# Optimization experiments

Measured on AMD Instinct MI355X. Metric: run time of the kernel, lower is better.

## Reference

```python
import jax, jax.numpy as jnp
import numpy as np

EPS = 1e-8
B, N, C, RBF = 2, 512, 32, 32  # batch, points (== neighbors), channels, rbf size
RI, RO, ORD = 3, 1, 3          # 2*rank_in+1, 2*rank_out+1, 2*order+1


def setup_inputs() -> dict:
    key = jax.random.key(0)
    k = jax.random.split(key, 5)
    tensor = jax.random.normal(k[0], (B, N, C, RI), dtype=jnp.float32)
    rbf = jax.random.uniform(k[1], (B, N, N, RBF), dtype=jnp.float32)
    rij = jax.random.normal(k[2], (B, N, N, 3), dtype=jnp.float32)
    # Radial MLP params: xavier-normal weights, zero biases (per Radial defaults)
    W1 = jax.random.normal(k[3], (C, RBF), dtype=jnp.float32) * float(np.sqrt(2.0 / (RBF + C)))
    W2 = jax.random.normal(k[4], (C, C), dtype=jnp.float32) * float(np.sqrt(2.0 / (C + C)))
    b1 = jnp.zeros((C,), jnp.float32)
    b2 = jnp.zeros((C,), jnp.float32)
    return dict(tensor=tensor, rbf=rbf, rij=rij, W1=W1, b1=b1, W2=W2, b2=b2)


def reference(tensor, rbf, rij, W1, b1, W2, b2):
    # Radial two-layer MLP applied per edge: [B,N,K,RBF] -> [B,N,K,C]
    hidden = jax.nn.relu(b1 + jnp.einsum('bnkl,ml->bnkm', rbf, W1))
    R = b2 + jnp.einsum('bnkl,ml->bnkm', hidden, W2)
    # Mask self/degenerate edges (order != 0): zero R where |rij| < EPS
    r2 = jnp.sum(rij * rij, axis=-1)                      # [B,N,K]
    R = jnp.where((jnp.sqrt(r2) < EPS)[..., None], jnp.zeros_like(R), R)
    # Spherical harmonic order 1: unit direction vectors (eps-stabilized norm)
    Y = rij / jnp.sqrt(jnp.maximum(r2, EPS))[..., None]   # [B,N,K,3]
    cg = jnp.eye(ORD, dtype=R.dtype).reshape(RO, ORD, RI)
    # Outer product radial x angular: [B,N,K,C,3]
    F_out = R[..., None] * Y[..., None, :]
    # Contract CG, filter, neighbor features; sums over neighbor axis c
    return jnp.einsum('ijk,abcdj,acdk->abdi', cg, F_out, tensor)  # [B,N,C,RO]
```

## Files before the change

### kernel.cpp

```cpp
#include <hip/hip_runtime.h>
#include <hip/hip_bf16.h>

using bf16x8 = __attribute__((ext_vector_type(8))) short;
using f32x4  = __attribute__((ext_vector_type(4))) float;
using f32x16 = __attribute__((ext_vector_type(16))) float;
using u32x4  = __attribute__((ext_vector_type(4))) unsigned;

constexpr int N_ = 512;

__device__ __forceinline__ unsigned pkbf(float lo, float hi) {
    unsigned a = (unsigned short)__builtin_bit_cast(short, __float2bfloat16(lo));
    unsigned b = (unsigned short)__builtin_bit_cast(short, __float2bfloat16(hi));
    return a | (b << 16);
}
__device__ __forceinline__ float bfhi2f(unsigned u) { return __builtin_bit_cast(float, u & 0xFFFF0000u); }
__device__ __forceinline__ float bflo2f(unsigned u) { return __builtin_bit_cast(float, u << 16); }
__device__ __forceinline__ void gl2lds16(const float* g, float* l) {
    __builtin_amdgcn_global_load_lds(
        (const __attribute__((address_space(1))) void*)g,
        (__attribute__((address_space(3))) void*)l, 16, 0, 0);
}

__global__ __launch_bounds__(256)
void pack_tensor(const float* __restrict__ tensor, unsigned* __restrict__ tw) {
    const int i = blockIdx.x * 256 + threadIdx.x;
    const float x = tensor[3 * i + 0];
    const float y = tensor[3 * i + 1];
    const float z = tensor[3 * i + 2];
    reinterpret_cast<uint2*>(tw)[i] = make_uint2(pkbf(x, y), pkbf(z, 0.f));
}

__global__ __launch_bounds__(256, 4)
void filter_D(const unsigned* __restrict__ tw,
              const float* __restrict__ rbf,
              const float* __restrict__ rij,
              const float* __restrict__ W1,
              const float* __restrict__ b1,
              const float* __restrict__ W2,
              const float* __restrict__ b2,
              float* __restrict__ out)
{
    const int bn   = blockIdx.x;
    const int b    = bn >> 9;
    const int tid  = threadIdx.x;
    const int lane = tid & 63;
    const int w    = tid >> 6;
    const int lam  = lane & 31;
    const int l5   = lane >> 5;

    __shared__ unsigned upk[N_][2];
    __shared__ float    red[4][32];

    const float* rij_bn = rij + (size_t)bn * (N_ * 3);
    const float* rbf_bn = rbf + (size_t)bn * (N_ * 32);
    const uint2* twb    = (const uint2*)tw + (size_t)b * (N_ * 32);

    #pragma unroll
    for (int t = 0; t < 2; ++t) {
        const int k = tid + t * 256;
        const float rx = rij_bn[3 * k + 0];
        const float ry = rij_bn[3 * k + 1];
        const float rz = rij_bn[3 * k + 2];
        const float r2 = rx * rx + ry * ry + rz * rz;
        const float inv = rsqrtf(fmaxf(r2, 1e-8f));
        const float sc = (r2 >= 1e-16f) ? inv : 0.f;
        upk[k][0] = pkbf(rx * sc, ry * sc);
        upk[k][1] = pkbf(rz * sc, 0.f);
    }

    bf16x8 W1b[2];
    {
        const float* p1 = W1 + lam * 32 + 8 * l5;
        const f32x4 a0 = ((const f32x4*)p1)[0], a1 = ((const f32x4*)p1)[1];
        const f32x4 a2 = ((const f32x4*)(p1 + 16))[0], a3 = ((const f32x4*)(p1 + 16))[1];
        #pragma unroll
        for (int e = 0; e < 4; ++e) {
            W1b[0][e]     = __builtin_bit_cast(short, __float2bfloat16(a0[e]));
            W1b[0][4 + e] = __builtin_bit_cast(short, __float2bfloat16(a1[e]));
            W1b[1][e]     = __builtin_bit_cast(short, __float2bfloat16(a2[e]));
            W1b[1][4 + e] = __builtin_bit_cast(short, __float2bfloat16(a3[e]));
        }
    }
    const float b1s = b1[lam];

    __syncthreads();

    f32x4 xa[2], xb[2], xc[2], xd[2];
    {
        const float* ap = rbf_bn + (size_t)(w * 128 + lam) * 32 + 8 * l5;
        xa[0] = ((const f32x4*)ap)[0];
        xb[0] = ((const f32x4*)ap)[1];
        xc[0] = ((const f32x4*)(ap + 16))[0];
        xd[0] = ((const f32x4*)(ap + 16))[1];
    }

    f32x16 G;
    #pragma unroll
    for (int i = 0; i < 16; ++i) G[i] = 0.f;
    float ssum = 0.f;

    #pragma unroll
    for (int j = 0; j < 4; ++j) {
        const int e0  = (w * 4 + j) * 32;
        const int cur = j & 1, nx = cur ^ 1;

        uint2 tv1[8], tv2[8];
        #pragma unroll
        for (int e = 0; e < 8; ++e) {
            const int k1 = e0 + 8 * l5 + e;
            tv1[e] = twb[k1 * 32 + lam];
            tv2[e] = twb[(k1 + 16) * 32 + lam];
        }

        bf16x8 X0, X1;
        #pragma unroll
        for (int e = 0; e < 4; ++e) {
            X0[e]     = __builtin_bit_cast(short, __float2bfloat16(xa[cur][e]));
            X0[4 + e] = __builtin_bit_cast(short, __float2bfloat16(xb[cur][e]));
            X1[e]     = __builtin_bit_cast(short, __float2bfloat16(xc[cur][e]));
            X1[4 + e] = __builtin_bit_cast(short, __float2bfloat16(xd[cur][e]));
        }
        if (j < 3) {
            const float* ap = rbf_bn + (size_t)(e0 + 32 + lam) * 32 + 8 * l5;
            xa[nx] = ((const f32x4*)ap)[0];
            xb[nx] = ((const f32x4*)ap)[1];
            xc[nx] = ((const f32x4*)(ap + 16))[0];
            xd[nx] = ((const f32x4*)(ap + 16))[1];
        }

        f32x16 h;
        #pragma unroll
        for (int i = 0; i < 16; ++i) h[i] = 0.f;
        h = __builtin_amdgcn_mfma_f32_32x32x16_bf16(X0, W1b[0], h, 0, 0, 0);
        h = __builtin_amdgcn_mfma_f32_32x32x16_bf16(X1, W1b[1], h, 0, 0, 0);

        unsigned P0, P1, P2, P3, P4, P5, P6, P7;
        {
            const float t0 = fmaxf(h[0] + b1s, 0.f),  t1v = fmaxf(h[1] + b1s, 0.f);
            const float t2v = fmaxf(h[2] + b1s, 0.f), t3 = fmaxf(h[3] + b1s, 0.f);
            const float t4 = fmaxf(h[4] + b1s, 0.f),  t5 = fmaxf(h[5] + b1s, 0.f);
            const float t6 = fmaxf(h[6] + b1s, 0.f),  t7 = fmaxf(h[7] + b1s, 0.f);
            const float t8 = fmaxf(h[8] + b1s, 0.f),  t9 = fmaxf(h[9] + b1s, 0.f);
            const float tA = fmaxf(h[10] + b1s, 0.f), tB = fmaxf(h[11] + b1s, 0.f);
            const float tC = fmaxf(h[12] + b1s, 0.f), tD = fmaxf(h[13] + b1s, 0.f);
            const float tE = fmaxf(h[14] + b1s, 0.f), tF = fmaxf(h[15] + b1s, 0.f);
            P0 = pkbf(t0, t1v); P1 = pkbf(t2v, t3);
            P2 = pkbf(t4, t5);  P3 = pkbf(t6, t7);
            P4 = pkbf(t8, t9);  P5 = pkbf(tA, tB);
            P6 = pkbf(tC, tD);  P7 = pkbf(tE, tF);
        }
        const unsigned Q0 = __shfl_xor(P0, 32, 64);
        const unsigned Q1 = __shfl_xor(P1, 32, 64);
        const unsigned Q2 = __shfl_xor(P2, 32, 64);
        const unsigned Q3 = __shfl_xor(P3, 32, 64);
        const unsigned Q4 = __shfl_xor(P4, 32, 64);
        const unsigned Q5 = __shfl_xor(P5, 32, 64);
        const unsigned Q6 = __shfl_xor(P6, 32, 64);
        const unsigned Q7 = __shfl_xor(P7, 32, 64);
        const bool lo = (l5 == 0);
        const u32x4 A1 = { lo ? P0 : Q2, lo ? P1 : Q3, lo ? Q0 : P2, lo ? Q1 : P3 };
        const u32x4 A2 = { lo ? P4 : Q6, lo ? P5 : Q7, lo ? Q4 : P6, lo ? Q5 : P7 };

        u32x4 B1d, B2d;
        float sp;
        #pragma unroll
        for (int e = 0; e < 8; ++e) {
            const int kl = 8 * l5 + e;
            const unsigned u0 = upk[e0 + kl][0], u1 = upk[e0 + kl][1];
            const float s = bflo2f(u0) * bflo2f(tv1[e].x) + bfhi2f(u0) * bfhi2f(tv1[e].x)
                          + bflo2f(u1) * bflo2f(tv1[e].y);
            ssum += s;
            if (e & 1) B1d[e >> 1] = pkbf(sp, s); else sp = s;
        }
        #pragma unroll
        for (int e = 0; e < 8; ++e) {
            const int kl = 16 + 8 * l5 + e;
            const unsigned u0 = upk[e0 + kl][0], u1 = upk[e0 + kl][1];
            const float s = bflo2f(u0) * bflo2f(tv2[e].x) + bfhi2f(u0) * bfhi2f(tv2[e].x)
                          + bflo2f(u1) * bflo2f(tv2[e].y);
            ssum += s;
            if (e & 1) B2d[e >> 1] = pkbf(sp, s); else sp = s;
        }

        G = __builtin_amdgcn_mfma_f32_32x32x16_bf16(
                __builtin_bit_cast(bf16x8, A1), __builtin_bit_cast(bf16x8, B1d), G, 0, 0, 0);
        G = __builtin_amdgcn_mfma_f32_32x32x16_bf16(
                __builtin_bit_cast(bf16x8, A2), __builtin_bit_cast(bf16x8, B2d), G, 0, 0, 0);
    }

    float p = 0.f;
    #pragma unroll
    for (int q = 0; q < 4; ++q) {
        const f32x4 wv = *(const f32x4*)(W2 + lam * 32 + 8 * q + 4 * l5);
        p += wv[0] * G[4 * q + 0] + wv[1] * G[4 * q + 1]
           + wv[2] * G[4 * q + 2] + wv[3] * G[4 * q + 3];
    }
    p    += __shfl_xor(p, 32, 64);
    ssum += __shfl_xor(ssum, 32, 64);
    const float o = p + b2[lam] * ssum;
    if (l5 == 0) red[w][lam] = o;
    __syncthreads();
    if (tid < 32)
        out[bn * 32 + tid] = red[0][tid] + red[1][tid] + red[2][tid] + red[3][tid];
}

__global__ __launch_bounds__(256, 4)
void filter_L(const float* __restrict__ tensor, const float* __restrict__ rbf,
              const float* __restrict__ rij, const float* __restrict__ W1,
              const float* __restrict__ b1, const float* __restrict__ W2,
              const float* __restrict__ b2, float* __restrict__ out)
{
    const int bn = blockIdx.x, b = bn >> 9, tid = threadIdx.x;
    const int lane = tid & 63, w = tid >> 6, lam = lane & 31, l5 = lane >> 5;
    __shared__ float Ts[4][3072];
    __shared__ unsigned upk[N_][2];
    __shared__ float red[4][32];
    const float* rij_bn = rij + (size_t)bn * (N_ * 3);
    const float* rbf_bn = rbf + (size_t)bn * (N_ * 32);
    const float* ten_b  = tensor + (size_t)b * (N_ * 32 * 3);
    #pragma unroll
    for (int t = 0; t < 2; ++t) {
        const int k = tid + t * 256;
        const float rx = rij_bn[3 * k], ry = rij_bn[3 * k + 1], rz = rij_bn[3 * k + 2];
        const float r2 = rx * rx + ry * ry + rz * rz;
        const float inv = rsqrtf(fmaxf(r2, 1e-8f));
        const float sc = (r2 >= 1e-16f) ? inv : 0.f;
        upk[k][0] = pkbf(rx * sc, ry * sc);
        upk[k][1] = pkbf(rz * sc, 0.f);
    }
    bf16x8 W1b[2];
    {
        const float* p1 = W1 + lam * 32 + 8 * l5;
        const f32x4 a0 = ((const f32x4*)p1)[0], a1 = ((const f32x4*)p1)[1];
        const f32x4 a2 = ((const f32x4*)(p1 + 16))[0], a3 = ((const f32x4*)(p1 + 16))[1];
        #pragma unroll
        for (int e = 0; e < 4; ++e) {
            W1b[0][e] = __builtin_bit_cast(short, __float2bfloat16(a0[e]));
            W1b[0][4 + e] = __builtin_bit_cast(short, __float2bfloat16(a1[e]));
            W1b[1][e] = __builtin_bit_cast(short, __float2bfloat16(a2[e]));
            W1b[1][4 + e] = __builtin_bit_cast(short, __float2bfloat16(a3[e]));
        }
    }
    const float b1s = b1[lam];
    __syncthreads();
    float* tsw = &Ts[w][0];
    f32x4 xa[2], xb[2], xc[2], xd[2];
    {
        const float* ap = rbf_bn + (size_t)(w * 128 + lam) * 32 + 8 * l5;
        xa[0] = ((const f32x4*)ap)[0]; xb[0] = ((const f32x4*)ap)[1];
        xc[0] = ((const f32x4*)(ap + 16))[0]; xd[0] = ((const f32x4*)(ap + 16))[1];
    }
    {
        const float* gsrc = ten_b + (size_t)(w * 128) * 96;
        #pragma unroll
        for (int it = 0; it < 12; ++it) gl2lds16(gsrc + it * 256 + lane * 4, tsw + it * 256);
    }
    f32x16 G;
    #pragma unroll
    for (int i = 0; i < 16; ++i) G[i] = 0.f;
    float ssum = 0.f;
    #pragma unroll
    for (int j = 0; j < 4; ++j) {
        const int e0 = (w * 4 + j) * 32, cur = j & 1, nx = cur ^ 1;
        bf16x8 X0, X1;
        #pragma unroll
        for (int e = 0; e < 4; ++e) {
            X0[e] = __builtin_bit_cast(short, __float2bfloat16(xa[cur][e]));
            X0[4 + e] = __builtin_bit_cast(short, __float2bfloat16(xb[cur][e]));
            X1[e] = __builtin_bit_cast(short, __float2bfloat16(xc[cur][e]));
            X1[4 + e] = __builtin_bit_cast(short, __float2bfloat16(xd[cur][e]));
        }
        if (j < 3) {
            const float* ap = rbf_bn + (size_t)(e0 + 32 + lam) * 32 + 8 * l5;
            xa[nx] = ((const f32x4*)ap)[0]; xb[nx] = ((const f32x4*)ap)[1];
            xc[nx] = ((const f32x4*)(ap + 16))[0]; xd[nx] = ((const f32x4*)(ap + 16))[1];
        }
        f32x16 h;
        #pragma unroll
        for (int i = 0; i < 16; ++i) h[i] = 0.f;
        h = __builtin_amdgcn_mfma_f32_32x32x16_bf16(X0, W1b[0], h, 0, 0, 0);
        h = __builtin_amdgcn_mfma_f32_32x32x16_bf16(X1, W1b[1], h, 0, 0, 0);
        unsigned P0, P1, P2, P3, P4, P5, P6, P7;
        {
            const float t0 = fmaxf(h[0] + b1s, 0.f), t1v = fmaxf(h[1] + b1s, 0.f);
            const float t2v = fmaxf(h[2] + b1s, 0.f), t3 = fmaxf(h[3] + b1s, 0.f);
            const float t4 = fmaxf(h[4] + b1s, 0.f), t5 = fmaxf(h[5] + b1s, 0.f);
            const float t6 = fmaxf(h[6] + b1s, 0.f), t7 = fmaxf(h[7] + b1s, 0.f);
            const float t8 = fmaxf(h[8] + b1s, 0.f), t9 = fmaxf(h[9] + b1s, 0.f);
            const float tA = fmaxf(h[10] + b1s, 0.f), tB = fmaxf(h[11] + b1s, 0.f);
            const float tC = fmaxf(h[12] + b1s, 0.f), tD = fmaxf(h[13] + b1s, 0.f);
            const float tE = fmaxf(h[14] + b1s, 0.f), tF = fmaxf(h[15] + b1s, 0.f);
            P0 = pkbf(t0, t1v); P1 = pkbf(t2v, t3); P2 = pkbf(t4, t5); P3 = pkbf(t6, t7);
            P4 = pkbf(t8, t9); P5 = pkbf(tA, tB); P6 = pkbf(tC, tD); P7 = pkbf(tE, tF);
        }
        const unsigned Q0 = __shfl_xor(P0, 32, 64), Q1 = __shfl_xor(P1, 32, 64);
        const unsigned Q2 = __shfl_xor(P2, 32, 64), Q3 = __shfl_xor(P3, 32, 64);
        const unsigned Q4 = __shfl_xor(P4, 32, 64), Q5 = __shfl_xor(P5, 32, 64);
        const unsigned Q6 = __shfl_xor(P6, 32, 64), Q7 = __shfl_xor(P7, 32, 64);
        const bool lo = (l5 == 0);
        const u32x4 A1 = { lo ? P0 : Q2, lo ? P1 : Q3, lo ? Q0 : P2, lo ? Q1 : P3 };
        const u32x4 A2 = { lo ? P4 : Q6, lo ? P5 : Q7, lo ? Q4 : P6, lo ? Q5 : P7 };
        if (j < 3) asm volatile("s_waitcnt vmcnt(4)" ::: "memory");
        else       asm volatile("s_waitcnt vmcnt(0)" ::: "memory");
        u32x4 B1d, B2d;
        float sp;
        #pragma unroll
        for (int e = 0; e < 8; ++e) {
            const int kl = 8 * l5 + e;
            const unsigned u0 = upk[e0 + kl][0], u1 = upk[e0 + kl][1];
            const float* tq = tsw + kl * 96 + 3 * lam;
            const float s = bflo2f(u0) * tq[0] + bfhi2f(u0) * tq[1] + bflo2f(u1) * tq[2];
            ssum += s;
            if (e & 1) B1d[e >> 1] = pkbf(sp, s); else sp = s;
        }
        #pragma unroll
        for (int e = 0; e < 8; ++e) {
            const int kl = 16 + 8 * l5 + e;
            const unsigned u0 = upk[e0 + kl][0], u1 = upk[e0 + kl][1];
            const float* tq = tsw + kl * 96 + 3 * lam;
            const float s = bflo2f(u0) * tq[0] + bfhi2f(u0) * tq[1] + bflo2f(u1) * tq[2];
            ssum += s;
            if (e & 1) B2d[e >> 1] = pkbf(sp, s); else sp = s;
        }
        asm volatile("s_waitcnt lgkmcnt(0)" ::: "memory");
        if (j < 3) {
            const float* gsrc = ten_b + (size_t)(e0 + 32) * 96;
            #pragma unroll
            for (int it = 0; it < 12; ++it) gl2lds16(gsrc + it * 256 + lane * 4, tsw + it * 256);
        }
        G = __builtin_amdgcn_mfma_f32_32x32x16_bf16(
                __builtin_bit_cast(bf16x8, A1), __builtin_bit_cast(bf16x8, B1d), G, 0, 0, 0);
        G = __builtin_amdgcn_mfma_f32_32x32x16_bf16(
                __builtin_bit_cast(bf16x8, A2), __builtin_bit_cast(bf16x8, B2d), G, 0, 0, 0);
    }
    float p = 0.f;
    #pragma unroll
    for (int q = 0; q < 4; ++q) {
        const f32x4 wv = *(const f32x4*)(W2 + lam * 32 + 8 * q + 4 * l5);
        p += wv[0] * G[4 * q + 0] + wv[1] * G[4 * q + 1]
           + wv[2] * G[4 * q + 2] + wv[3] * G[4 * q + 3];
    }
    p    += __shfl_xor(p, 32, 64);
    ssum += __shfl_xor(ssum, 32, 64);
    const float o = p + b2[lam] * ssum;
    if (l5 == 0) red[w][lam] = o;
    __syncthreads();
    if (tid < 32)
        out[bn * 32 + tid] = red[0][tid] + red[1][tid] + red[2][tid] + red[3][tid];
}

extern "C" void kernel_launch(void* const* d_in, const int* in_sizes, int n_in,
                              void* d_out, int out_size, void* d_ws, size_t ws_size,
                              hipStream_t stream) {
    const float* tensor = (const float*)d_in[0];
    const float* rbf    = (const float*)d_in[1];
    const float* rij    = (const float*)d_in[2];
    const float* W1     = (const float*)d_in[3];
    const float* b1     = (const float*)d_in[4];
    const float* W2     = (const float*)d_in[5];
    const float* b2     = (const float*)d_in[6];
    float* out = (float*)d_out;

    const size_t ws_need = (size_t)2 * N_ * 32 * 2 * sizeof(unsigned);
    dim3 block(256), grid(2 * N_);
    if (ws_size >= ws_need) {
        unsigned* tw = (unsigned*)d_ws;
        pack_tensor<<<dim3(256), block, 0, stream>>>(tensor, tw);
        filter_D<<<grid, block, 0, stream>>>(tw, rbf, rij, W1, b1, W2, b2, out);
    } else {
        filter_L<<<grid, block, 0, stream>>>(tensor, rbf, rij, W1, b1, W2, b2, out);
    }
}
```

Baseline: 30.60 us.

## Stage rbf tiles through swizzled LDS with async global-to-LDS double buffering

```diff
diff --git a/kernel.cpp b/kernel.cpp
--- a/kernel.cpp
+++ b/kernel.cpp
@@ -31,7 +31,7 @@
 }
 
 __global__ __launch_bounds__(256, 4)
-void filter_D(const unsigned* __restrict__ tw,
+void filter_S(const unsigned* __restrict__ tw,
               const float* __restrict__ rbf,
               const float* __restrict__ rij,
               const float* __restrict__ W1,
@@ -48,11 +48,12 @@
     const int lam  = lane & 31;
     const int l5   = lane >> 5;
 
+    __shared__ float    rbf_s[4][2][1024];
     __shared__ unsigned upk[N_][2];
     __shared__ float    red[4][32];
 
     const float* rij_bn = rij + (size_t)bn * (N_ * 3);
-    const float* rbf_bn = rbf + (size_t)bn * (N_ * 32);
+    const char*  rbf_bc = (const char*)(rbf + (size_t)bn * (N_ * 32));
     const uint2* twb    = (const uint2*)tw + (size_t)b * (N_ * 32);
 
     #pragma unroll
@@ -85,14 +86,17 @@
 
     __syncthreads();
 
-    f32x4 xa[2], xb[2], xc[2], xd[2];
-    {
-        const float* ap = rbf_bn + (size_t)(w * 128 + lam) * 32 + 8 * l5;
-        xa[0] = ((const f32x4*)ap)[0];
-        xb[0] = ((const f32x4*)ap)[1];
-        xc[0] = ((const f32x4*)(ap + 16))[0];
-        xd[0] = ((const f32x4*)(ap + 16))[1];
-    }
+    const int soff = (lane * 16) ^ (((lane >> 3) & 7) << 4);
+
+    auto stage = [&](int t, int bufi) {
+        const char* tb = rbf_bc + (size_t)(w * 4 + t) * 4096;
+        float* dst = &rbf_s[w][bufi][0];
+        #pragma unroll
+        for (int it = 0; it < 4; ++it)
+            gl2lds16((const float*)(tb + it * 1024 + soff), dst + it * 256);
+    };
+
+    stage(0, 0);
 
     f32x16 G;
     #pragma unroll
@@ -101,8 +105,7 @@
 
     #pragma unroll
     for (int j = 0; j < 4; ++j) {
-        const int e0  = (w * 4 + j) * 32;
-        const int cur = j & 1, nx = cur ^ 1;
+        const int e0 = (w * 4 + j) * 32;
 
         uint2 tv1[8], tv2[8];
         #pragma unroll
@@ -111,21 +114,29 @@
             tv1[e] = twb[k1 * 32 + lam];
             tv2[e] = twb[(k1 + 16) * 32 + lam];
         }
-
+        __builtin_amdgcn_sched_barrier(0);
+
+        if (j < 3) stage(j + 1, (j + 1) & 1);
+        __builtin_amdgcn_sched_barrier(0);
+
+        if (j < 3) asm volatile("s_waitcnt vmcnt(20)" ::: "memory");
+        else       asm volatile("s_waitcnt vmcnt(16)" ::: "memory");
+        __builtin_amdgcn_sched_barrier(0);
+
+        const char* bufc = (const char*)&rbf_s[w][j & 1][0];
+        const int   lin  = lam * 128 + l5 * 32;
+        const int   sw   = (lam & 7) << 4;
+        const f32x4 xa = *(const f32x4*)(bufc + ((lin +  0) ^ sw));
+        const f32x4 xb = *(const f32x4*)(bufc + ((lin + 16) ^ sw));
+        const f32x4 xc = *(const f32x4*)(bufc + ((lin + 64) ^ sw));
+        const f32x4 xd = *(const f32x4*)(bufc + ((lin + 80) ^ sw));
         bf16x8 X0, X1;
         #pragma unroll
         for (int e = 0; e < 4; ++e) {
-            X0[e]     = __builtin_bit_cast(short, __float2bfloat16(xa[cur][e]));
-            X0[4 + e] = __builtin_bit_cast(short, __float2bfloat16(xb[cur][e]));
-            X1[e]     = __builtin_bit_cast(short, __float2bfloat16(xc[cur][e]));
-            X1[4 + e] = __builtin_bit_cast(short, __float2bfloat16(xd[cur][e]));
-        }
-        if (j < 3) {
-            const float* ap = rbf_bn + (size_t)(e0 + 32 + lam) * 32 + 8 * l5;
-            xa[nx] = ((const f32x4*)ap)[0];
-            xb[nx] = ((const f32x4*)ap)[1];
-            xc[nx] = ((const f32x4*)(ap + 16))[0];
-            xd[nx] = ((const f32x4*)(ap + 16))[1];
+            X0[e]     = __builtin_bit_cast(short, __float2bfloat16(xa[e]));
+            X0[4 + e] = __builtin_bit_cast(short, __float2bfloat16(xb[e]));
+            X1[e]     = __builtin_bit_cast(short, __float2bfloat16(xc[e]));
+            X1[4 + e] = __builtin_bit_cast(short, __float2bfloat16(xd[e]));
         }
 
         f32x16 h;
@@ -366,7 +377,7 @@
     if (ws_size >= ws_need) {
         unsigned* tw = (unsigned*)d_ws;
         pack_tensor<<<dim3(256), block, 0, stream>>>(tensor, tw);
-        filter_D<<<grid, block, 0, stream>>>(tw, rbf, rij, W1, b1, W2, b2, out);
+        filter_S<<<grid, block, 0, stream>>>(tw, rbf, rij, W1, b1, W2, b2, out);
     } else {
         filter_L<<<grid, block, 0, stream>>>(tensor, rbf, rij, W1, b1, W2, b2, out);
     }
```

Result: faster. 28.72 us (-6.2%).
